# Kernel tuning notes

Measured on AMD Instinct MI355X. Metric: run time of the kernel, lower is better.

## Reference

```python
import jax, jax.numpy as jnp
import numpy as np

DIM = 1024
DEPTH = 4
D_STATE = 16
D_CONV = 4
D_INNER = 2 * DIM
DT_RANK = (DIM + 15) // 16  # 64, ceil(dim/16) as in mamba-ssm
B_SZ, L = 4, 2048


def setup_inputs() -> dict:
    key = jax.random.key(0)
    ks = jax.random.split(key, 10)
    s = 0.02
    x = jax.random.normal(ks[0], (B_SZ, L, DIM), jnp.float32)
    in_proj_w = jax.random.normal(ks[1], (DEPTH, 2 * D_INNER, DIM), jnp.float32) * s
    conv_w = jax.random.normal(ks[2], (DEPTH, D_INNER, D_CONV), jnp.float32) * 0.2
    conv_b = jnp.zeros((DEPTH, D_INNER), jnp.float32)
    x_proj_w = jax.random.normal(ks[3], (DEPTH, DT_RANK + 2 * D_STATE, D_INNER), jnp.float32) * s
    dt_proj_w = jax.random.normal(ks[4], (DEPTH, D_INNER, DT_RANK), jnp.float32) * s
    # bias init so softplus(bias) ~ 0.01 (mamba dt_init)
    dt_proj_b = jnp.full((DEPTH, D_INNER), float(np.log(np.expm1(0.01))), jnp.float32)
    # S4D-real init: A = -(1..d_state)
    A_log = jnp.broadcast_to(jnp.log(jnp.arange(1, D_STATE + 1, dtype=jnp.float32)), (D_INNER, D_STATE))
    A_log = jnp.broadcast_to(A_log, (DEPTH, D_INNER, D_STATE))
    D = jnp.ones((DEPTH, D_INNER), jnp.float32)
    out_proj_w = jax.random.normal(ks[5], (DEPTH, DIM, D_INNER), jnp.float32) * s
    return {"x": x, "in_proj_w": in_proj_w, "conv_w": conv_w, "conv_b": conv_b,
            "x_proj_w": x_proj_w, "dt_proj_w": dt_proj_w, "dt_proj_b": dt_proj_b,
            "A_log": A_log, "D": D, "out_proj_w": out_proj_w}


def _selective_scan(u, delta, A, Bm, Cm, D):
    # u, delta: [B, L, d_inner]; Bm, Cm: [B, L, d_state]; A: [d_inner, d_state]
    def step(h, inp):
        u_t, d_t, b_t, c_t = inp  # [B,di], [B,di], [B,ds], [B,ds]
        dA = jnp.exp(d_t[:, :, None] * A)                 # [B,di,ds]
        h = dA * h + (d_t * u_t)[:, :, None] * b_t[:, None, :]
        y = jnp.einsum('bds,bs->bd', h, c_t)
        return h, y

    h0 = jnp.zeros((u.shape[0], u.shape[2], A.shape[1]), u.dtype)
    xs = (u.transpose(1, 0, 2), delta.transpose(1, 0, 2),
          Bm.transpose(1, 0, 2), Cm.transpose(1, 0, 2))
    _, ys = jax.lax.scan(step, h0, xs)                     # ys: [L,B,di]
    return ys.transpose(1, 0, 2) + u * D


def _mamba_layer(x, in_w, cw, cb, xp_w, dtw, dtb, A_log, D, ow):
    xz = jnp.einsum('bld,ed->ble', x, in_w)               # [B,L,2*di]
    xi, z = jnp.split(xz, 2, axis=-1)
    # causal depthwise conv over L
    xc = jax.lax.conv_general_dilated(
        xi.transpose(0, 2, 1),                             # [B,di,L]
        cw[:, None, :],                                    # [di,1,k]
        window_strides=(1,), padding=[(D_CONV - 1, 0)],
        feature_group_count=D_INNER,
        dimension_numbers=('NCH', 'OIH', 'NCH'))
    xc = jax.nn.silu(xc.transpose(0, 2, 1) + cb)           # [B,L,di]
    dbc = jnp.einsum('bld,ed->ble', xc, xp_w)              # [B,L,dt_rank+2*ds]
    dt, Bm, Cm = jnp.split(dbc, [DT_RANK, DT_RANK + D_STATE], axis=-1)
    delta = jax.nn.softplus(jnp.einsum('blr,dr->bld', dt, dtw) + dtb)
    A = -jnp.exp(A_log)
    y = _selective_scan(xc, delta, A, Bm, Cm, D)
    y = y * jax.nn.silu(z)
    return jnp.einsum('bld,od->blo', y, ow)


def reference(x, in_proj_w, conv_w, conv_b, x_proj_w, dt_proj_w, dt_proj_b, A_log, D, out_proj_w):
    for i in range(DEPTH):
        x = _mamba_layer(x, in_proj_w[i], conv_w[i], conv_b[i], x_proj_w[i],
                         dt_proj_w[i], dt_proj_b[i], A_log[i], D[i], out_proj_w[i])
    return x
```

## Files before the change

kernel.cpp:

```cpp
#include <hip/hip_runtime.h>
#include <hip/hip_bf16.h>
#include <math.h>

#define DIMK 1024
#define NDEPTH 4
#define DS 16
#define DCONV 4
#define DI 2048
#define DTR 64
#define NB 4
#define SL 2048
#define MT (NB * SL)
#define NXZ (2 * DI)
#define NDBC (DTR + 2 * DS)

typedef float f32x4 __attribute__((ext_vector_type(4)));
typedef short short8 __attribute__((ext_vector_type(8)));
typedef short short4v __attribute__((ext_vector_type(4)));

__device__ inline unsigned short f2bf(float f) {
    unsigned u = __builtin_bit_cast(unsigned, f);
    unsigned r = (u + 0x7FFFu + ((u >> 16) & 1u)) >> 16;
    return (unsigned short)r;
}
__device__ inline float bf2f(unsigned short h) {
    unsigned u = ((unsigned)h) << 16;
    return __builtin_bit_cast(float, u);
}
__device__ inline void split_bf(float f, unsigned short& hi, unsigned short& lo) {
    hi = f2bf(f);
    lo = f2bf(f - bf2f(hi));
}
__device__ inline unsigned short cvt1(float f) {
    __hip_bfloat16 t = __float2bfloat16(f);
    return __builtin_bit_cast(unsigned short, t);
}
__device__ inline void mfma16(f32x4& d, short8 a, short8 b) {
    asm volatile("v_mfma_f32_16x16x32_bf16 %0, %1, %2, %0"
                 : "+v"(d) : "v"(a), "v"(b));
}
__device__ __forceinline__ float dpp_sum16(float p) {
    asm("v_add_f32_dpp %0, %0, %0 quad_perm:[1,0,3,2] row_mask:0xf bank_mask:0xf bound_ctrl:0" : "+v"(p));
    asm("v_add_f32_dpp %0, %0, %0 quad_perm:[2,3,0,1] row_mask:0xf bank_mask:0xf bound_ctrl:0" : "+v"(p));
    asm("v_add_f32_dpp %0, %0, %0 row_ror:4 row_mask:0xf bank_mask:0xf bound_ctrl:0" : "+v"(p));
    asm("v_add_f32_dpp %0, %0, %0 row_ror:8 row_mask:0xf bank_mask:0xf bound_ctrl:0" : "+v"(p));
    return p;
}
__device__ __forceinline__ float exp2_raw(float x) {
    float r;
    asm("v_exp_f32 %0, %1" : "=v"(r) : "v"(x));
    return r;
}
__device__ __forceinline__ void gload16(const unsigned short* g, unsigned short* l) {
    __builtin_amdgcn_global_load_lds(
        (const __attribute__((address_space(1))) unsigned int*)(g),
        (__attribute__((address_space(3))) unsigned int*)(l),
        16, 0, 0);
}

__global__ __launch_bounds__(256) void cvt_bf16(
    const float* __restrict__ s, unsigned short* __restrict__ d, int n4)
{
    const int g = blockIdx.x * 256 + threadIdx.x;
    if (g < n4) {
        const float4 f = *(const float4*)(s + (size_t)g * 4);
        short4v v;
        v[0] = (short)cvt1(f.x); v[1] = (short)cvt1(f.y);
        v[2] = (short)cvt1(f.z); v[3] = (short)cvt1(f.w);
        *(short4v*)(d + (size_t)g * 4) = v;
    }
}

__global__ __launch_bounds__(256) void cvt_layer(
    const float* __restrict__ wi, const float* __restrict__ owp,
    const float* __restrict__ dtwp, const float* __restrict__ xpwp,
    unsigned short* __restrict__ wi16, unsigned short* __restrict__ ow16,
    unsigned short* __restrict__ dtwh, unsigned short* __restrict__ dtwl,
    unsigned short* __restrict__ xpwh, unsigned short* __restrict__ xpwl,
    int fastd, int fastx)
{
    int g = blockIdx.x * 256 + threadIdx.x;
    const int n4w = NXZ * DIMK / 4;
    const int n4o = DIMK * DI / 4;
    const int n4d = DI * DTR / 4;
    const int n4x = NDBC * DI / 4;
    if (g < n4w) {
        const float4 f = *(const float4*)(wi + (size_t)g * 4);
        short4v v;
        v[0] = (short)cvt1(f.x); v[1] = (short)cvt1(f.y);
        v[2] = (short)cvt1(f.z); v[3] = (short)cvt1(f.w);
        *(short4v*)(wi16 + (size_t)g * 4) = v;
        return;
    }
    g -= n4w;
    if (g < n4o) {
        const float4 f = *(const float4*)(owp + (size_t)g * 4);
        short4v v;
        v[0] = (short)cvt1(f.x); v[1] = (short)cvt1(f.y);
        v[2] = (short)cvt1(f.z); v[3] = (short)cvt1(f.w);
        *(short4v*)(ow16 + (size_t)g * 4) = v;
        return;
    }
    g -= n4o;
    if (g < n4d) {
        if (fastd) {
            const float4 f = *(const float4*)(dtwp + (size_t)g * 4);
            short4v h4, l4;
            #pragma unroll
            for (int e = 0; e < 4; ++e) {
                unsigned short h, l;
                split_bf((&f.x)[e], h, l);
                h4[e] = (short)h; l4[e] = (short)l;
            }
            *(short4v*)(dtwh + (size_t)g * 4) = h4;
            *(short4v*)(dtwl + (size_t)g * 4) = l4;
        }
        return;
    }
    g -= n4d;
    if (g < n4x && fastx) {
        const float4 f = *(const float4*)(xpwp + (size_t)g * 4);
        short4v h4, l4;
        #pragma unroll
        for (int e = 0; e < 4; ++e) {
            unsigned short h, l;
            split_bf((&f.x)[e], h, l);
            h4[e] = (short)h; l4[e] = (short)l;
        }
        *(short4v*)(xpwh + (size_t)g * 4) = h4;
        *(short4v*)(xpwl + (size_t)g * 4) = l4;
    }
}

__global__ __launch_bounds__(256) void cvt_all(
    const float* __restrict__ wi, const float* __restrict__ owp,
    const float* __restrict__ dtwp, const float* __restrict__ xpwp,
    unsigned short* __restrict__ wi16, unsigned short* __restrict__ ow16,
    unsigned short* __restrict__ dtwh, unsigned short* __restrict__ dtwl,
    unsigned short* __restrict__ xpwh, unsigned short* __restrict__ xpwl)
{
    const int n4w = NXZ * DIMK / 4;
    const int n4o = DIMK * DI / 4;
    const int n4d = DI * DTR / 4;
    const int n4x = NDBC * DI / 4;
    const int per = n4w + n4o + n4d + n4x;
    int g = blockIdx.x * 256 + threadIdx.x;
    const int ly = g / per;
    if (ly >= NDEPTH) return;
    g -= ly * per;
    if (g < n4w) {
        const float4 f = *(const float4*)(wi + (size_t)ly * NXZ * DIMK + (size_t)g * 4);
        short4v v;
        v[0] = (short)cvt1(f.x); v[1] = (short)cvt1(f.y);
        v[2] = (short)cvt1(f.z); v[3] = (short)cvt1(f.w);
        *(short4v*)(wi16 + (size_t)ly * NXZ * DIMK + (size_t)g * 4) = v;
        return;
    }
    g -= n4w;
    if (g < n4o) {
        const float4 f = *(const float4*)(owp + (size_t)ly * DIMK * DI + (size_t)g * 4);
        short4v v;
        v[0] = (short)cvt1(f.x); v[1] = (short)cvt1(f.y);
        v[2] = (short)cvt1(f.z); v[3] = (short)cvt1(f.w);
        *(short4v*)(ow16 + (size_t)ly * DIMK * DI + (size_t)g * 4) = v;
        return;
    }
    g -= n4o;
    if (g < n4d) {
        const float4 f = *(const float4*)(dtwp + (size_t)ly * DI * DTR + (size_t)g * 4);
        short4v h4, l4;
        #pragma unroll
        for (int e = 0; e < 4; ++e) {
            unsigned short h, l;
            split_bf((&f.x)[e], h, l);
            h4[e] = (short)h; l4[e] = (short)l;
        }
        *(short4v*)(dtwh + (size_t)ly * DI * DTR + (size_t)g * 4) = h4;
        *(short4v*)(dtwl + (size_t)ly * DI * DTR + (size_t)g * 4) = l4;
        return;
    }
    g -= n4d;
    if (g < n4x) {
        const float4 f = *(const float4*)(xpwp + (size_t)ly * NDBC * DI + (size_t)g * 4);
        short4v h4, l4;
        #pragma unroll
        for (int e = 0; e < 4; ++e) {
            unsigned short h, l;
            split_bf((&f.x)[e], h, l);
            h4[e] = (short)h; l4[e] = (short)l;
        }
        *(short4v*)(xpwh + (size_t)ly * NDBC * DI + (size_t)g * 4) = h4;
        *(short4v*)(xpwl + (size_t)ly * NDBC * DI + (size_t)g * 4) = l4;
    }
}

template <int CBF>
__global__ __launch_bounds__(256) void gemm_bb(
    const unsigned short* __restrict__ A, const unsigned short* __restrict__ B,
    void* __restrict__ Cv, int K, int lda, int ldb, int ldc)
{
    __shared__ unsigned short As[128 * 32];
    __shared__ unsigned short Bs[128 * 32];
    int id = blockIdx.y * gridDim.x + blockIdx.x;
    const int qq = (gridDim.x * gridDim.y) >> 3;
    id = (id & 7) * qq + (id >> 3);
    const int bm = (id / gridDim.x) * 128, bn = (id % gridDim.x) * 128;

    const int tid = threadIdx.x;
    const int wv = tid >> 6, ln = tid & 63;
    const int wr = wv >> 1, wc = wv & 1;
    const int fr = ln & 15, kg = ln >> 4;
    const int sr0 = wv * 32 + (ln >> 2);
    const int sr1 = sr0 + 16;
    const int sl = ln & 3;
    const int cg0 = sl ^ ((sr0 >> 1) & 3);
    const int cg1 = sl ^ ((sr1 >> 1) & 3);
    const unsigned short* pa0 = A + (size_t)(bm + sr0) * lda + cg0 * 8;
    const unsigned short* pa1 = A + (size_t)(bm + sr1) * lda + cg1 * 8;
    const unsigned short* pb0 = B + (size_t)(bn + sr0) * ldb + cg0 * 8;
    const unsigned short* pb1 = B + (size_t)(bn + sr1) * ldb + cg1 * 8;
    unsigned short* la0 = As + (wv * 32 + 0) * 32;
    unsigned short* la1 = As + (wv * 32 + 16) * 32;
    unsigned short* lb0 = Bs + (wv * 32 + 0) * 32;
    unsigned short* lb1 = Bs + (wv * 32 + 16) * 32;
    int offA[4], offB[4];
    #pragma unroll
    for (int f = 0; f < 4; ++f) {
        const int ra = wr * 64 + f * 16 + fr;
        offA[f] = ra * 32 + ((kg ^ ((ra >> 1) & 3)) * 8);
        const int rb = wc * 64 + f * 16 + fr;
        offB[f] = rb * 32 + ((kg ^ ((rb >> 1) & 3)) * 8);
    }
    f32x4 acc[4][4] = {};
    for (int k0 = 0; k0 < K; k0 += 32) {
        gload16(pa0 + k0, la0);
        gload16(pa1 + k0, la1);
        gload16(pb0 + k0, lb0);
        gload16(pb1 + k0, lb1);
        __syncthreads();
        short8 af[4], bw[4];
        #pragma unroll
        for (int f = 0; f < 4; ++f) {
            af[f] = *(const short8*)&As[offA[f]];
            bw[f] = *(const short8*)&Bs[offB[f]];
        }
        #pragma unroll
        for (int fi = 0; fi < 4; ++fi)
            #pragma unroll
            for (int fj = 0; fj < 4; ++fj)
                mfma16(acc[fi][fj], af[fi], bw[fj]);
        __syncthreads();
    }
    #pragma unroll
    for (int fi = 0; fi < 4; ++fi) {
        const int m0 = bm + wr * 64 + fi * 16 + kg * 4;
        #pragma unroll
        for (int fj = 0; fj < 4; ++fj) {
            const int n = bn + wc * 64 + fj * 16 + fr;
            #pragma unroll
            for (int q = 0; q < 4; ++q) {
                if (CBF) {
                    unsigned short* Cs = (unsigned short*)Cv;
                    Cs[(size_t)(m0 + q) * ldc + n] = cvt1(acc[fi][fj][q]);
                } else {
                    float* Cf = (float*)Cv;
                    Cf[(size_t)(m0 + q) * ldc + n] = acc[fi][fj][q];
                }
            }
        }
    }
}

template <int CBF>
__global__ __launch_bounds__(256) void gemm_fb(
    const float* __restrict__ A, const unsigned short* __restrict__ B,
    void* __restrict__ Cv, int K, int lda, int ldb, int ldc)
{
    __shared__ unsigned short As[2][128 * 32];
    __shared__ unsigned short Bs[2][128 * 32];
    int id = blockIdx.y * gridDim.x + blockIdx.x;
    const int qq = (gridDim.x * gridDim.y) >> 3;
    id = (id & 7) * qq + (id >> 3);
    const int bm = (id / gridDim.x) * 128, bn = (id % gridDim.x) * 128;

    const int tid = threadIdx.x;
    const int wv = tid >> 6, ln = tid & 63;
    const int wr = wv >> 1, wc = wv & 1;
    const int fr = ln & 15, kg = ln >> 4;
    const int r = tid >> 1, hf = tid & 1;
    const int sr0 = wv * 32 + (ln >> 2);
    const int sr1 = sr0 + 16;
    const int sl = ln & 3;
    const int cg0 = sl ^ ((sr0 >> 1) & 3);
    const int cg1 = sl ^ ((sr1 >> 1) & 3);
    const unsigned short* pb0 = B + (size_t)(bn + sr0) * ldb + cg0 * 8;
    const unsigned short* pb1 = B + (size_t)(bn + sr1) * ldb + cg1 * 8;
    const int ldst0 = (wv * 32 + 0) * 32;
    const int ldst1 = (wv * 32 + 16) * 32;
    const float* ga = A + (size_t)(bm + r) * lda + hf * 16;
    const int pk0 = (2 * hf + 0) ^ ((r >> 1) & 3);
    const int pk1 = (2 * hf + 1) ^ ((r >> 1) & 3);
    int offA[4], offB[4];
    #pragma unroll
    for (int f = 0; f < 4; ++f) {
        const int ra = wr * 64 + f * 16 + fr;
        offA[f] = ra * 32 + ((kg ^ ((ra >> 1) & 3)) * 8);
        const int rb = wc * 64 + f * 16 + fr;
        offB[f] = rb * 32 + ((kg ^ ((rb >> 1) & 3)) * 8);
    }
    f32x4 acc[4][4] = {};
    {
        float4 f0 = *(const float4*)(ga + 0);
        float4 f1 = *(const float4*)(ga + 4);
        float4 f2 = *(const float4*)(ga + 8);
        float4 f3 = *(const float4*)(ga + 12);
        short8 v;
        v[0] = (short)cvt1(f0.x); v[1] = (short)cvt1(f0.y);
        v[2] = (short)cvt1(f0.z); v[3] = (short)cvt1(f0.w);
        v[4] = (short)cvt1(f1.x); v[5] = (short)cvt1(f1.y);
        v[6] = (short)cvt1(f1.z); v[7] = (short)cvt1(f1.w);
        *(short8*)&As[0][r * 32 + pk0 * 8] = v;
        v[0] = (short)cvt1(f2.x); v[1] = (short)cvt1(f2.y);
        v[2] = (short)cvt1(f2.z); v[3] = (short)cvt1(f2.w);
        v[4] = (short)cvt1(f3.x); v[5] = (short)cvt1(f3.y);
        v[6] = (short)cvt1(f3.z); v[7] = (short)cvt1(f3.w);
        *(short8*)&As[0][r * 32 + pk1 * 8] = v;
        gload16(pb0, &Bs[0][ldst0]);
        gload16(pb1, &Bs[0][ldst1]);
    }
    __syncthreads();
    int cur = 0;
    for (int k0 = 0; k0 < K; k0 += 32) {
        const int nxt = cur ^ 1;
        const bool more = (k0 + 32 < K);
        float4 f0, f1, f2, f3;
        if (more) {
            gload16(pb0 + k0 + 32, &Bs[nxt][ldst0]);
            gload16(pb1 + k0 + 32, &Bs[nxt][ldst1]);
            f0 = *(const float4*)(ga + k0 + 32);
            f1 = *(const float4*)(ga + k0 + 36);
            f2 = *(const float4*)(ga + k0 + 40);
            f3 = *(const float4*)(ga + k0 + 44);
        }
        short8 af[4], bw[4];
        #pragma unroll
        for (int f = 0; f < 4; ++f) {
            af[f] = *(const short8*)&As[cur][offA[f]];
            bw[f] = *(const short8*)&Bs[cur][offB[f]];
        }
        #pragma unroll
        for (int fi = 0; fi < 4; ++fi)
            #pragma unroll
            for (int fj = 0; fj < 4; ++fj)
                mfma16(acc[fi][fj], af[fi], bw[fj]);
        if (more) {
            short8 v;
            v[0] = (short)cvt1(f0.x); v[1] = (short)cvt1(f0.y);
            v[2] = (short)cvt1(f0.z); v[3] = (short)cvt1(f0.w);
            v[4] = (short)cvt1(f1.x); v[5] = (short)cvt1(f1.y);
            v[6] = (short)cvt1(f1.z); v[7] = (short)cvt1(f1.w);
            *(short8*)&As[nxt][r * 32 + pk0 * 8] = v;
            v[0] = (short)cvt1(f2.x); v[1] = (short)cvt1(f2.y);
            v[2] = (short)cvt1(f2.z); v[3] = (short)cvt1(f2.w);
            v[4] = (short)cvt1(f3.x); v[5] = (short)cvt1(f3.y);
            v[6] = (short)cvt1(f3.z); v[7] = (short)cvt1(f3.w);
            *(short8*)&As[nxt][r * 32 + pk1 * 8] = v;
        }
        __syncthreads();
        cur = nxt;
    }
    #pragma unroll
    for (int fi = 0; fi < 4; ++fi) {
        const int m0 = bm + wr * 64 + fi * 16 + kg * 4;
        #pragma unroll
        for (int fj = 0; fj < 4; ++fj) {
            const int n = bn + wc * 64 + fj * 16 + fr;
            #pragma unroll
            for (int q = 0; q < 4; ++q) {
                if (CBF) {
                    unsigned short* Cs = (unsigned short*)Cv;
                    Cs[(size_t)(m0 + q) * ldc + n] = cvt1(acc[fi][fj][q]);
                } else {
                    float* Cf = (float*)Cv;
                    Cf[(size_t)(m0 + q) * ldc + n] = acc[fi][fj][q];
                }
            }
        }
    }
}

__global__ __launch_bounds__(256) void gemm_mfma(
    const float* __restrict__ A, const float* __restrict__ W,
    float* __restrict__ C, int K, int lda, int ldc)
{
    __shared__ unsigned short As[128 * 32];
    __shared__ unsigned short Ws[128 * 32];
    const int tid = threadIdx.x;
    const int bm = blockIdx.y * 128;
    const int bn = blockIdx.x * 128;
    const int r = tid >> 1;
    const int h = tid & 1;
    const int wv = tid >> 6;
    const int wr = wv >> 1;
    const int wc = wv & 1;
    const int ln = tid & 63;
    const int fr = ln & 15;
    const int kg = ln >> 4;
    f32x4 acc[4][4] = {};
    const float* ga = A + (size_t)(bm + r) * lda + h * 16;
    const float* gw = W + (size_t)(bn + r) * K + h * 16;
    for (int k0 = 0; k0 < K; k0 += 32) {
        #pragma unroll
        for (int p = 0; p < 2; ++p) {
            const int pk = (2 * h + p) ^ ((r >> 1) & 3);
            float4 f0 = *(const float4*)(ga + k0 + p * 8);
            float4 f1 = *(const float4*)(ga + k0 + p * 8 + 4);
            short8 v;
            v[0] = (short)cvt1(f0.x); v[1] = (short)cvt1(f0.y);
            v[2] = (short)cvt1(f0.z); v[3] = (short)cvt1(f0.w);
            v[4] = (short)cvt1(f1.x); v[5] = (short)cvt1(f1.y);
            v[6] = (short)cvt1(f1.z); v[7] = (short)cvt1(f1.w);
            *(short8*)&As[r * 32 + pk * 8] = v;
            f0 = *(const float4*)(gw + k0 + p * 8);
            f1 = *(const float4*)(gw + k0 + p * 8 + 4);
            v[0] = (short)cvt1(f0.x); v[1] = (short)cvt1(f0.y);
            v[2] = (short)cvt1(f0.z); v[3] = (short)cvt1(f0.w);
            v[4] = (short)cvt1(f1.x); v[5] = (short)cvt1(f1.y);
            v[6] = (short)cvt1(f1.z); v[7] = (short)cvt1(f1.w);
            *(short8*)&Ws[r * 32 + pk * 8] = v;
        }
        __syncthreads();
        short8 af[4], bw[4];
        #pragma unroll
        for (int f = 0; f < 4; ++f) {
            const int ra = wr * 64 + f * 16 + fr;
            af[f] = *(const short8*)&As[ra * 32 + ((kg ^ ((ra >> 1) & 3)) * 8)];
            const int rb = wc * 64 + f * 16 + fr;
            bw[f] = *(const short8*)&Ws[rb * 32 + ((kg ^ ((rb >> 1) & 3)) * 8)];
        }
        #pragma unroll
        for (int fi = 0; fi < 4; ++fi)
            #pragma unroll
            for (int fj = 0; fj < 4; ++fj)
                mfma16(acc[fi][fj], af[fi], bw[fj]);
        __syncthreads();
    }
    #pragma unroll
    for (int fi = 0; fi < 4; ++fi) {
        const int m0 = bm + wr * 64 + fi * 16 + kg * 4;
        #pragma unroll
        for (int fj = 0; fj < 4; ++fj) {
            const int n = bn + wc * 64 + fj * 16 + fr;
            #pragma unroll
            for (int q = 0; q < 4; ++q)
                C[(size_t)(m0 + q) * ldc + n] = acc[fi][fj][q];
        }
    }
}

__global__ __launch_bounds__(256) void gemm_xproj_pre(
    const unsigned short* __restrict__ Ahg, const unsigned short* __restrict__ Alg,
    const unsigned short* __restrict__ Whg, const unsigned short* __restrict__ Wlg,
    float* __restrict__ C,
    unsigned short* __restrict__ dth, unsigned short* __restrict__ dtl)
{
    __shared__ unsigned short Ahs[2][128 * 32], Als[2][128 * 32];
    __shared__ unsigned short Whs[2][32 * 32], Wls[2][32 * 32];
    int id = blockIdx.y * gridDim.x + blockIdx.x;
    const int qq = (gridDim.x * gridDim.y) >> 3;
    id = (id & 7) * qq + (id >> 3);
    const int bm = (id / gridDim.x) * 128, bn = (id % gridDim.x) * 32;

    const int tid = threadIdx.x;
    const int wv = tid >> 6, ln = tid & 63;
    const int fr = ln & 15, kg = ln >> 4;
    const int sr0 = wv * 32 + (ln >> 2);
    const int sr1 = sr0 + 16;
    const int sl = ln & 3;
    const int cg0 = sl ^ ((sr0 >> 1) & 3);
    const int cg1 = sl ^ ((sr1 >> 1) & 3);
    const unsigned short* pah0 = Ahg + (size_t)(bm + sr0) * DI + cg0 * 8;
    const unsigned short* pah1 = Ahg + (size_t)(bm + sr1) * DI + cg1 * 8;
    const unsigned short* pal0 = Alg + (size_t)(bm + sr0) * DI + cg0 * 8;
    const unsigned short* pal1 = Alg + (size_t)(bm + sr1) * DI + cg1 * 8;
    const int lA0 = (wv * 32 + 0) * 32;
    const int lA1 = (wv * 32 + 16) * 32;
    const int wrow = (wv & 1) * 16 + (ln >> 2);
    const int cgw = sl ^ ((wrow >> 1) & 3);
    const unsigned short* pw = ((wv < 2) ? Whg : Wlg) + (size_t)(bn + wrow) * DI + cgw * 8;
    const int lW = ((wv & 1) * 16) * 32;
    unsigned short* wdst[2];
    wdst[0] = (wv < 2) ? &Whs[0][lW] : &Wls[0][lW];
    wdst[1] = (wv < 2) ? &Whs[1][lW] : &Wls[1][lW];

    int offA[2], offW[2];
    #pragma unroll
    for (int f = 0; f < 2; ++f) {
        const int ra = wv * 32 + f * 16 + fr;
        offA[f] = ra * 32 + ((kg ^ ((ra >> 1) & 3)) * 8);
        const int rb = f * 16 + fr;
        offW[f] = rb * 32 + ((kg ^ ((rb >> 1) & 3)) * 8);
    }
    f32x4 acc[2][2] = {};
    gload16(pah0, &Ahs[0][lA0]);
    gload16(pah1, &Ahs[0][lA1]);
    gload16(pal0, &Als[0][lA0]);
    gload16(pal1, &Als[0][lA1]);
    gload16(pw, wdst[0]);
    __syncthreads();
    int cur = 0;
    for (int k0 = 0; k0 < DI; k0 += 32) {
        const int nxt = cur ^ 1;
        if (k0 + 32 < DI) {
            gload16(pah0 + k0 + 32, &Ahs[nxt][lA0]);
            gload16(pah1 + k0 + 32, &Ahs[nxt][lA1]);
            gload16(pal0 + k0 + 32, &Als[nxt][lA0]);
            gload16(pal1 + k0 + 32, &Als[nxt][lA1]);
            gload16(pw + k0 + 32, wdst[nxt]);
        }
        short8 ah[2], alo[2], bh[2], bl[2];
        #pragma unroll
        for (int f = 0; f < 2; ++f) {
            ah[f]  = *(const short8*)&Ahs[cur][offA[f]];
            alo[f] = *(const short8*)&Als[cur][offA[f]];
            bh[f]  = *(const short8*)&Whs[cur][offW[f]];
            bl[f]  = *(const short8*)&Wls[cur][offW[f]];
        }
        #pragma unroll
        for (int fi = 0; fi < 2; ++fi)
            #pragma unroll
            for (int fj = 0; fj < 2; ++fj) {
                mfma16(acc[fi][fj], ah[fi], bh[fj]);
                mfma16(acc[fi][fj], ah[fi], bl[fj]);
                mfma16(acc[fi][fj], alo[fi], bh[fj]);
            }
        __syncthreads();
        cur = nxt;
    }
    #pragma unroll
    for (int fi = 0; fi < 2; ++fi) {
        const int m0 = bm + wv * 32 + fi * 16 + kg * 4;
        #pragma unroll
        for (int fj = 0; fj < 2; ++fj) {
            const int n = bn + fj * 16 + fr;
            #pragma unroll
            for (int q = 0; q < 4; ++q) {
                const float v = acc[fi][fj][q];
                C[(size_t)(m0 + q) * NDBC + n] = v;
                if (n < DTR) {
                    unsigned short hh, llo;
                    split_bf(v, hh, llo);
                    dth[(size_t)(m0 + q) * DTR + n] = hh;
                    dtl[(size_t)(m0 + q) * DTR + n] = llo;
                }
            }
        }
    }
}

template <int WRDT>
__global__ __launch_bounds__(256) void gemm_xproj(
    const float* __restrict__ A, const float* __restrict__ W,
    float* __restrict__ C, int K, int lda,
    unsigned short* __restrict__ dth, unsigned short* __restrict__ dtl)
{
    __shared__ unsigned short Ah[128 * 32], Al[128 * 32];
    __shared__ unsigned short Wh[32 * 32], Wl[32 * 32];
    const int tid = threadIdx.x;
    const int bm = blockIdx.y * 128;
    const int bn = blockIdx.x * 32;
    const int r = tid >> 1, hf = tid & 1;
    const int wv = tid >> 6;
    const int ln = tid & 63, fr = ln & 15, kg = ln >> 4;
    const int wsr = tid >> 3;
    const int wc4 = (tid & 7) << 2;
    f32x4 acc[2][2] = {};
    const float* ga = A + (size_t)(bm + r) * lda + hf * 16;
    const float* gw = W + (size_t)(bn + wsr) * K + wc4;
    for (int k0 = 0; k0 < K; k0 += 32) {
        #pragma unroll
        for (int j = 0; j < 4; ++j) {
            const int col = hf * 16 + j * 4;
            const int ad = r * 32 + (((col >> 3) ^ ((r >> 1) & 3)) << 3) + (col & 7);
            const float4 fa = *(const float4*)(ga + k0 + j * 4);
            short4v h4, l4;
            #pragma unroll
            for (int e = 0; e < 4; ++e) {
                unsigned short hh, llo;
                split_bf((&fa.x)[e], hh, llo);
                h4[e] = (short)hh; l4[e] = (short)llo;
            }
            *(short4v*)&Ah[ad] = h4;
            *(short4v*)&Al[ad] = l4;
        }
        {
            const int ad = wsr * 32 + (((wc4 >> 3) ^ ((wsr >> 1) & 3)) << 3) + (wc4 & 7);
            const float4 fw = *(const float4*)(gw + k0);
            short4v h4, l4;
            #pragma unroll
            for (int e = 0; e < 4; ++e) {
                unsigned short hh, llo;
                split_bf((&fw.x)[e], hh, llo);
                h4[e] = (short)hh; l4[e] = (short)llo;
            }
            *(short4v*)&Wh[ad] = h4;
            *(short4v*)&Wl[ad] = l4;
        }
        __syncthreads();
        short8 ah[2], alo[2], bh[2], bl[2];
        #pragma unroll
        for (int f = 0; f < 2; ++f) {
            const int ra = wv * 32 + f * 16 + fr;
            const int ao = ra * 32 + ((kg ^ ((ra >> 1) & 3)) * 8);
            ah[f]  = *(const short8*)&Ah[ao];
            alo[f] = *(const short8*)&Al[ao];
            const int rb = f * 16 + fr;
            const int bo = rb * 32 + ((kg ^ ((rb >> 1) & 3)) * 8);
            bh[f] = *(const short8*)&Wh[bo];
            bl[f] = *(const short8*)&Wl[bo];
        }
        #pragma unroll
        for (int fi = 0; fi < 2; ++fi)
            #pragma unroll
            for (int fj = 0; fj < 2; ++fj) {
                mfma16(acc[fi][fj], ah[fi], bh[fj]);
                mfma16(acc[fi][fj], ah[fi], bl[fj]);
                mfma16(acc[fi][fj], alo[fi], bh[fj]);
            }
        __syncthreads();
    }
    #pragma unroll
    for (int fi = 0; fi < 2; ++fi) {
        const int m0 = bm + wv * 32 + fi * 16 + kg * 4;
        #pragma unroll
        for (int fj = 0; fj < 2; ++fj) {
            const int n = bn + fj * 16 + fr;
            #pragma unroll
            for (int q = 0; q < 4; ++q) {
                const float v = acc[fi][fj][q];
                C[(size_t)(m0 + q) * NDBC + n] = v;
                if (WRDT && n < DTR) {
                    unsigned short hh, llo;
                    split_bf(v, hh, llo);
                    dth[(size_t)(m0 + q) * DTR + n] = hh;
                    dtl[(size_t)(m0 + q) * DTR + n] = llo;
                }
            }
        }
    }
}

__global__ __launch_bounds__(256) void gemm_delta(
    const float* __restrict__ A, const float* __restrict__ W,
    float* __restrict__ C, const float* __restrict__ bias)
{
    __shared__ unsigned short Ah[128 * 32], Al[128 * 32];
    __shared__ unsigned short Wh[128 * 32], Wl[128 * 32];
    const int tid = threadIdx.x;
    const int bm = blockIdx.y * 128;
    const int bn = blockIdx.x * 128;
    const int r = tid >> 1, hf = tid & 1;
    const int wv = tid >> 6, wr = wv >> 1, wc = wv & 1;
    const int ln = tid & 63, fr = ln & 15, kg = ln >> 4;
    f32x4 acc[4][4] = {};
    const float* ga = A + (size_t)(bm + r) * NDBC + hf * 16;
    const float* gw = W + (size_t)(bn + r) * DTR + hf * 16;
    for (int k0 = 0; k0 < DTR; k0 += 32) {
        #pragma unroll
        for (int j = 0; j < 4; ++j) {
            const int col = hf * 16 + j * 4;
            const int ad = r * 32 + (((col >> 3) ^ ((r >> 1) & 3)) << 3) + (col & 7);
            const float4 fa = *(const float4*)(ga + k0 + j * 4);
            const float4 fw = *(const float4*)(gw + k0 + j * 4);
            short4v ah4, al4, wh4, wl4;
            #pragma unroll
            for (int e = 0; e < 4; ++e) {
                unsigned short hh, llo;
                split_bf((&fa.x)[e], hh, llo);
                ah4[e] = (short)hh; al4[e] = (short)llo;
                split_bf((&fw.x)[e], hh, llo);
                wh4[e] = (short)hh; wl4[e] = (short)llo;
            }
            *(short4v*)&Ah[ad] = ah4; *(short4v*)&Al[ad] = al4;
            *(short4v*)&Wh[ad] = wh4; *(short4v*)&Wl[ad] = wl4;
        }
        __syncthreads();
        short8 ah[4], alo[4], bh[4], bl[4];
        #pragma unroll
        for (int f = 0; f < 4; ++f) {
            const int ra = wr * 64 + f * 16 + fr;
            const int ao = ra * 32 + ((kg ^ ((ra >> 1) & 3)) * 8);
            ah[f]  = *(const short8*)&Ah[ao];
            alo[f] = *(const short8*)&Al[ao];
            const int rb = wc * 64 + f * 16 + fr;
            const int bo = rb * 32 + ((kg ^ ((rb >> 1) & 3)) * 8);
            bh[f] = *(const short8*)&Wh[bo];
            bl[f] = *(const short8*)&Wl[bo];
        }
        #pragma unroll
        for (int fi = 0; fi < 4; ++fi)
            #pragma unroll
            for (int fj = 0; fj < 4; ++fj) {
                mfma16(acc[fi][fj], ah[fi], bh[fj]);
                mfma16(acc[fi][fj], ah[fi], bl[fj]);
                mfma16(acc[fi][fj], alo[fi], bh[fj]);
            }
        __syncthreads();
    }
    #pragma unroll
    for (int fi = 0; fi < 4; ++fi) {
        const int m0 = bm + wr * 64 + fi * 16 + kg * 4;
        #pragma unroll
        for (int fj = 0; fj < 4; ++fj) {
            const int n = bn + wc * 64 + fj * 16 + fr;
            const float bb = bias[n];
            #pragma unroll
            for (int q = 0; q < 4; ++q) {
                float v = acc[fi][fj][q] + bb;
                v = (v > 20.f) ? v : log1pf(__expf(v));
                C[(size_t)(m0 + q) * NXZ + n] = v;
            }
        }
    }
}

__global__ __launch_bounds__(256) void gemm_delta_pre(
    const unsigned short* __restrict__ Ahg, const unsigned short* __restrict__ Alg,
    const unsigned short* __restrict__ Whg, const unsigned short* __restrict__ Wlg,
    float* __restrict__ C, const float* __restrict__ bias)
{
    __shared__ unsigned short sAh[128 * 64], sAl[128 * 64];
    __shared__ unsigned short sWh[128 * 64], sWl[128 * 64];
    const int tid = threadIdx.x;
    const int bm = blockIdx.y * 128;
    const int bn = blockIdx.x * 128;
    const int wv = tid >> 6, ln = tid & 63;
    const int wr = wv >> 1, wc = wv & 1;
    const int fr = ln & 15, kg = ln >> 4;
    const int srow = ln >> 3;
    const int g = ln & 7;
    const int half = g >> 2, sub = g & 3;
    #pragma unroll
    for (int j = 0; j < 4; ++j) {
        const int row = wv * 32 + j * 8 + srow;
        const int sub2 = sub ^ ((row >> 1) & 3);
        const int scol = half * 32 + sub2 * 8;
        const int dst = (wv * 32 + j * 8) * 64;
        gload16(Ahg + (size_t)(bm + row) * DTR + scol, sAh + dst);
        gload16(Alg + (size_t)(bm + row) * DTR + scol, sAl + dst);
        gload16(Whg + (size_t)(bn + row) * DTR + scol, sWh + dst);
        gload16(Wlg + (size_t)(bn + row) * DTR + scol, sWl + dst);
    }
    __syncthreads();
    f32x4 acc[4][4] = {};
    #pragma unroll
    for (int ks = 0; ks < 2; ++ks) {
        short8 ah[4], alo[4], bh[4], bl[4];
        #pragma unroll
        for (int f = 0; f < 4; ++f) {
            const int ra = wr * 64 + f * 16 + fr;
            const int ao = ra * 64 + ks * 32 + ((kg ^ ((ra >> 1) & 3)) * 8);
            ah[f]  = *(const short8*)&sAh[ao];
            alo[f] = *(const short8*)&sAl[ao];
            const int rb = wc * 64 + f * 16 + fr;
            const int bo = rb * 64 + ks * 32 + ((kg ^ ((rb >> 1) & 3)) * 8);
            bh[f] = *(const short8*)&sWh[bo];
            bl[f] = *(const short8*)&sWl[bo];
        }
        #pragma unroll
        for (int fi = 0; fi < 4; ++fi)
            #pragma unroll
            for (int fj = 0; fj < 4; ++fj) {
                mfma16(acc[fi][fj], ah[fi], bh[fj]);
                mfma16(acc[fi][fj], ah[fi], bl[fj]);
                mfma16(acc[fi][fj], alo[fi], bh[fj]);
            }
    }
    #pragma unroll
    for (int fi = 0; fi < 4; ++fi) {
        const int m0 = bm + wr * 64 + fi * 16 + kg * 4;
        #pragma unroll
        for (int fj = 0; fj < 4; ++fj) {
            const int n = bn + wc * 64 + fj * 16 + fr;
            const float bb = bias[n];
            #pragma unroll
            for (int q = 0; q < 4; ++q) {
                float v = acc[fi][fj][q] + bb;
                v = (v > 20.f) ? v : log1pf(__expf(v));
                C[(size_t)(m0 + q) * NXZ + n] = v;
            }
        }
    }
}

__global__ __launch_bounds__(256) void conv_silu(
    const float* __restrict__ xz, const float* __restrict__ cw,
    const float* __restrict__ cb, float* __restrict__ xc)
{
    const int g = blockIdx.x * 256 + threadIdx.x;
    const int c4 = g & (DI / 4 - 1);
    const int mq = g >> 9;
    const int m0 = mq << 2;
    const int l0 = m0 & (SL - 1);
    const int c = c4 << 2;
    const float4 w0 = *(const float4*)(cw + (size_t)(c + 0) * DCONV);
    const float4 w1 = *(const float4*)(cw + (size_t)(c + 1) * DCONV);
    const float4 w2 = *(const float4*)(cw + (size_t)(c + 2) * DCONV);
    const float4 w3 = *(const float4*)(cw + (size_t)(c + 3) * DCONV);
    const float4 cb4 = *(const float4*)(cb + c);
    float4 x[7];
    #pragma unroll
    for (int i = 0; i < 7; ++i) {
        if (l0 - 3 + i >= 0)
            x[i] = *(const float4*)(xz + (size_t)(m0 - 3 + i) * NXZ + c);
        else
            x[i] = make_float4(0.f, 0.f, 0.f, 0.f);
    }
    #pragma unroll
    for (int j = 0; j < 4; ++j) {
        float4 acc = cb4;
        #pragma unroll
        for (int k = 0; k < DCONV; ++k) {
            const float4 v = x[j + k];
            acc.x = fmaf(v.x, (&w0.x)[k], acc.x);
            acc.y = fmaf(v.y, (&w1.x)[k], acc.y);
            acc.z = fmaf(v.z, (&w2.x)[k], acc.z);
            acc.w = fmaf(v.w, (&w3.x)[k], acc.w);
        }
        acc.x = acc.x / (1.f + __expf(-acc.x));
        acc.y = acc.y / (1.f + __expf(-acc.y));
        acc.z = acc.z / (1.f + __expf(-acc.z));
        acc.w = acc.w / (1.f + __expf(-acc.w));
        *(float4*)(xc + (size_t)(m0 + j) * DI + c) = acc;
    }
}

__global__ __launch_bounds__(256) void conv_silu_split(
    const float* __restrict__ xz, const float* __restrict__ cw,
    const float* __restrict__ cb, unsigned short* __restrict__ xch,
    unsigned short* __restrict__ xcl)
{
    const int g = blockIdx.x * 256 + threadIdx.x;
    const int c4 = g & (DI / 4 - 1);
    const int mq = g >> 9;
    const int m0 = mq << 2;
    const int l0 = m0 & (SL - 1);
    const int c = c4 << 2;
    const float4 w0 = *(const float4*)(cw + (size_t)(c + 0) * DCONV);
    const float4 w1 = *(const float4*)(cw + (size_t)(c + 1) * DCONV);
    const float4 w2 = *(const float4*)(cw + (size_t)(c + 2) * DCONV);
    const float4 w3 = *(const float4*)(cw + (size_t)(c + 3) * DCONV);
    const float4 cb4 = *(const float4*)(cb + c);
    float4 x[7];
    #pragma unroll
    for (int i = 0; i < 7; ++i) {
        if (l0 - 3 + i >= 0)
            x[i] = *(const float4*)(xz + (size_t)(m0 - 3 + i) * NXZ + c);
        else
            x[i] = make_float4(0.f, 0.f, 0.f, 0.f);
    }
    #pragma unroll
    for (int j = 0; j < 4; ++j) {
        float4 acc = cb4;
        #pragma unroll
        for (int k = 0; k < DCONV; ++k) {
            const float4 v = x[j + k];
            acc.x = fmaf(v.x, (&w0.x)[k], acc.x);
            acc.y = fmaf(v.y, (&w1.x)[k], acc.y);
            acc.z = fmaf(v.z, (&w2.x)[k], acc.z);
            acc.w = fmaf(v.w, (&w3.x)[k], acc.w);
        }
        short4v h4, l4;
        #pragma unroll
        for (int e = 0; e < 4; ++e) {
            float a = (&acc.x)[e];
            a = a / (1.f + __expf(-a));
            unsigned short hh, llo;
            split_bf(a, hh, llo);
            h4[e] = (short)hh; l4[e] = (short)llo;
        }
        *(short4v*)(xch + (size_t)(m0 + j) * DI + c) = h4;
        *(short4v*)(xcl + (size_t)(m0 + j) * DI + c) = l4;
    }
}

template <int YBF, int UBF>
__global__ __launch_bounds__(256) void scan_k(
    const float* uf, const unsigned short* __restrict__ uh,
    const unsigned short* __restrict__ ul,
    const float* __restrict__ dbc,
    const float* __restrict__ xz, void* __restrict__ yv,
    const float* __restrict__ Alog, const float* __restrict__ Dl)
{
    const int b = blockIdx.y;
    const int c0 = blockIdx.x * 16;
    const int tid = threadIdx.x;
    const int ch = tid >> 4;
    const int s = tid & 15;
    const float Aa = -__expf(Alog[(size_t)(c0 + ch) * DS + s]) * 1.44269504088896f;
    __shared__ float sdl[2][16][68];
    __shared__ float sxb[2][16][68];
    __shared__ float sbc[2][32][68];
    __shared__ float sy[2][64][16];
    __shared__ float sD[16];
    if (tid < 16) sD[tid] = Dl[c0 + tid];
    float h = 0.f;
    const int row = tid >> 2;
    const int q = (tid & 3) << 2;
    const size_t base = (size_t)b * SL;
    const int r2a = tid >> 3, q2a = (tid & 7) << 2;
    const int r2b = 32 + (tid >> 3);

    float4 dlv, zv, g0, g1, uvf;
    short4v uh4, ul4;
    {
        const size_t m = base + row;
        dlv = *(const float4*)(xz + m * NXZ + c0 + q);
        if (UBF) {
            uh4 = *(const short4v*)(uh + m * DI + c0 + q);
            ul4 = *(const short4v*)(ul + m * DI + c0 + q);
        } else {
            uvf = *(const float4*)(uf + m * DI + c0 + q);
        }
        zv = *(const float4*)(xz + m * NXZ + DI + c0 + q);
        g0 = *(const float4*)(dbc + (base + r2a) * NDBC + DTR + q2a);
        g1 = *(const float4*)(dbc + (base + r2b) * NDBC + DTR + q2a);
    }
    float4 p0c, p1c, p0p, p1p;
    int pp = 0;
    __syncthreads();
    const int NT = SL / 64;
    for (int tile = 0; tile < NT; ++tile) {
        const int buf = tile & 1;
        float4 uv;
        if (UBF) {
            #pragma unroll
            for (int e = 0; e < 4; ++e)
                (&uv.x)[e] = bf2f((unsigned short)uh4[e]) +
                             bf2f((unsigned short)ul4[e]);
        } else uv = uvf;
        #pragma unroll
        for (int j = 0; j < 4; ++j) {
            const float dl = (&dlv.x)[j], uu = (&uv.x)[j], zz = (&zv.x)[j];
            const float w = zz / (1.f + __expf(-zz));
            sdl[buf][q + j][row] = dl;
            sxb[buf][q + j][row] = dl * uu;
            (&p1c.x)[j] = w;
            (&p0c.x)[j] = uu * sD[q + j] * w;
        }
        sbc[buf][q2a + 0][r2a] = g0.x; sbc[buf][q2a + 1][r2a] = g0.y;
        sbc[buf][q2a + 2][r2a] = g0.z; sbc[buf][q2a + 3][r2a] = g0.w;
        sbc[buf][q2a + 0][r2b] = g1.x; sbc[buf][q2a + 1][r2b] = g1.y;
        sbc[buf][q2a + 2][r2b] = g1.z; sbc[buf][q2a + 3][r2b] = g1.w;
        __syncthreads();
        if (tile > 0) {
            const size_t mp = base + (size_t)(tile - 1) * 64 + row;
            if (YBF) {
                unsigned short* y16 = (unsigned short*)yv;
                short4v s4;
                #pragma unroll
                for (int e = 0; e < 4; ++e)
                    s4[e] = (short)cvt1(fmaf(sy[pp ^ 1][row][q + e],
                                             (&p1p.x)[e], (&p0p.x)[e]));
                *(short4v*)(y16 + mp * DI + c0 + q) = s4;
            } else {
                float* y = (float*)yv;
                float4 yvv;
                #pragma unroll
                for (int e = 0; e < 4; ++e)
                    (&yvv.x)[e] = fmaf(sy[pp ^ 1][row][q + e],
                                       (&p1p.x)[e], (&p0p.x)[e]);
                *(float4*)(y + mp * DI + c0 + q) = yvv;
            }
        }
        if (tile + 1 < NT) {
            const size_t m = base + (size_t)(tile + 1) * 64 + row;
            dlv = *(const float4*)(xz + m * NXZ + c0 + q);
            if (UBF) {
                uh4 = *(const short4v*)(uh + m * DI + c0 + q);
                ul4 = *(const short4v*)(ul + m * DI + c0 + q);
            } else {
                uvf = *(const float4*)(uf + m * DI + c0 + q);
            }
            zv = *(const float4*)(xz + m * NXZ + DI + c0 + q);
            const size_t mb2 = base + (size_t)(tile + 1) * 64;
            g0 = *(const float4*)(dbc + (mb2 + r2a) * NDBC + DTR + q2a);
            g1 = *(const float4*)(dbc + (mb2 + r2b) * NDBC + DTR + q2a);
        }
        for (int it = 0; it < 16; ++it) {
            const int t0 = it * 4;
            const float4 dl4 = *(const float4*)&sdl[buf][ch][t0];
            const float4 xb4 = *(const float4*)&sxb[buf][ch][t0];
            const float4 B4  = *(const float4*)&sbc[buf][s][t0];
            const float4 C4  = *(const float4*)&sbc[buf][16 + s][t0];
            float py0, py1, py2, py3;
            {
                const float dA = exp2_raw(dl4.x * Aa);
                h = fmaf(dA, h, xb4.x * B4.x);
                py0 = dpp_sum16(h * C4.x);
            }
            {
                const float dA = exp2_raw(dl4.y * Aa);
                h = fmaf(dA, h, xb4.y * B4.y);
                py1 = dpp_sum16(h * C4.y);
            }
            {
                const float dA = exp2_raw(dl4.z * Aa);
                h = fmaf(dA, h, xb4.z * B4.z);
                py2 = dpp_sum16(h * C4.z);
            }
            {
                const float dA = exp2_raw(dl4.w * Aa);
                h = fmaf(dA, h, xb4.w * B4.w);
                py3 = dpp_sum16(h * C4.w);
            }
            if (s < 4) {
                const int t = t0 + s;
                const float lo_ = (s & 1) ? py1 : py0;
                const float hi_ = (s & 1) ? py3 : py2;
                sy[pp][t][ch] = (s & 2) ? hi_ : lo_;
            }
        }
        p0p = p0c; p1p = p1c;
        pp ^= 1;
    }
    __syncthreads();
    {
        const size_t mp = base + (size_t)(NT - 1) * 64 + row;
        if (YBF) {
            unsigned short* y16 = (unsigned short*)yv;
            short4v s4;
            #pragma unroll
            for (int e = 0; e < 4; ++e)
                s4[e] = (short)cvt1(fmaf(sy[pp ^ 1][row][q + e],
                                         (&p1p.x)[e], (&p0p.x)[e]));
            *(short4v*)(y16 + mp * DI + c0 + q) = s4;
        } else {
            float* y = (float*)yv;
            float4 yvv;
            #pragma unroll
            for (int e = 0; e < 4; ++e)
                (&yvv.x)[e] = fmaf(sy[pp ^ 1][row][q + e],
                                   (&p1p.x)[e], (&p0p.x)[e]);
            *(float4*)(y + mp * DI + c0 + q) = yvv;
        }
    }
}

extern "C" void kernel_launch(void* const* d_in, const int* in_sizes, int n_in,
                              void* d_out, int out_size, void* d_ws, size_t ws_size,
                              hipStream_t stream)
{
    const float* x0   = (const float*)d_in[0];
    const float* in_w = (const float*)d_in[1];
    const float* cw   = (const float*)d_in[2];
    const float* cb   = (const float*)d_in[3];
    const float* xpw  = (const float*)d_in[4];
    const float* dtw  = (const float*)d_in[5];
    const float* dtb  = (const float*)d_in[6];
    const float* Alog = (const float*)d_in[7];
    const float* Dp   = (const float*)d_in[8];
    const float* ow   = (const float*)d_in[9];

    const size_t perB = (size_t)SL * (NXZ + DI + NDBC) * sizeof(float);
    const size_t wby  = ((size_t)NXZ * DIMK + (size_t)DIMK * DI) * 2;
    int nbc = 0, fast = 0;
    if (ws_size >= 4 * perB + wby)      { nbc = 4; fast = 1; }
    else if (ws_size >= 2 * perB + wby) { nbc = 2; fast = 1; }
    else if (ws_size >= perB + wby)     { nbc = 1; fast = 1; }
    else if (ws_size >= 4 * perB)       { nbc = 4; }
    else if (ws_size >= 2 * perB)       { nbc = 2; }
    else if (ws_size >= perB)           { nbc = 1; }
    else return;
    const int nchunks = NB / nbc;
    const int M = nbc * SL;
    const size_t dtby = ((size_t)DI * DTR * 2 + (size_t)M * DTR * 2) * 2;
    const size_t yby  = (size_t)M * DI * 2;
    const size_t xpby = (size_t)NDBC * DI * 2 * 2;
    const size_t base = (size_t)nbc * perB + wby;
    const int fastd = fast && (ws_size >= base + dtby);
    const int fasty = fastd && (ws_size >= base + dtby + yby);
    const int fastx = fasty && (ws_size >= base + dtby + yby + xpby);
    const size_t wAll = ((size_t)NDEPTH * NXZ * DIMK + (size_t)NDEPTH * DIMK * DI +
                         2 * (size_t)NDEPTH * DI * DTR + 2 * (size_t)NDEPTH * NDBC * DI) * 2;
    const size_t chunkBy = (size_t)nbc * perB;
    const int fastw = fastx &&
        (ws_size >= chunkBy + wAll + (size_t)M * DTR * 2 * 2 + yby);

    float* xz  = (float*)d_ws;
    float* xc  = xz + (size_t)M * NXZ;
    float* dbc = xc + (size_t)M * DI;
    unsigned short* xch = (unsigned short*)xc;
    unsigned short* xcl = xch + (size_t)M * DI;

    unsigned short* p = (unsigned short*)(dbc + (size_t)M * NDBC);
    unsigned short *wi16, *ow16, *dtwh, *dtwl, *xpwh, *xpwl, *dth, *dtl, *y16;
    size_t wiStride = 0, owStride = 0, dtwStride = 0, xpwStride = 0;
    if (fastw) {
        wi16 = p;                    p += (size_t)NDEPTH * NXZ * DIMK;
        ow16 = p;                    p += (size_t)NDEPTH * DIMK * DI;
        dtwh = p;                    p += (size_t)NDEPTH * DI * DTR;
        dtwl = p;                    p += (size_t)NDEPTH * DI * DTR;
        xpwh = p;                    p += (size_t)NDEPTH * NDBC * DI;
        xpwl = p;                    p += (size_t)NDEPTH * NDBC * DI;
        wiStride = (size_t)NXZ * DIMK; owStride = (size_t)DIMK * DI;
        dtwStride = (size_t)DI * DTR;  xpwStride = (size_t)NDBC * DI;
    } else {
        wi16 = p;                    p += (size_t)NXZ * DIMK;
        ow16 = p;                    p += (size_t)DIMK * DI;
        dtwh = p;                    p += (size_t)DI * DTR;
        dtwl = p;                    p += (size_t)DI * DTR;
        xpwh = nullptr; xpwl = nullptr;
    }
    dth = p;                         p += (size_t)M * DTR;
    dtl = p;                         p += (size_t)M * DTR;
    y16 = p;                         p += (size_t)M * DI;
    if (!fastw && fastx) { xpwh = p; p += (size_t)NDBC * DI; xpwl = p; }

    unsigned short* xb16 = (unsigned short*)d_out + (size_t)MT * DIMK;
    float* xbuf = (float*)d_out;

    const dim3 blk(256);
    if (fastx) {
        const int n4x0 = MT * DIMK / 4;
        cvt_bf16<<<dim3(n4x0 / 256), blk, 0, stream>>>(x0, xb16, n4x0);
    }
    if (fastw) {
        const int per = (NXZ * DIMK / 4) + (DIMK * DI / 4) + (DI * DTR / 4) +
                        (NDBC * DI / 4);
        cvt_all<<<dim3((NDEPTH * per + 255) / 256), blk, 0, stream>>>(
            in_w, ow, dtw, xpw, wi16, ow16, dtwh, dtwl, xpwh, xpwl);
    }
    const int ncv = (NXZ * DIMK / 4) + (DIMK * DI / 4) + (DI * DTR / 4) +
                    (NDBC * DI / 4);
    for (int ly = 0; ly < NDEPTH; ++ly) {
        const float* Wi   = in_w + (size_t)ly * NXZ * DIMK;
        const float* cwl  = cw   + (size_t)ly * DI * DCONV;
        const float* cbl  = cb   + (size_t)ly * DI;
        const float* xpl  = xpw  + (size_t)ly * NDBC * DI;
        const float* dtwl_ = dtw + (size_t)ly * DI * DTR;
        const float* dtbl = dtb  + (size_t)ly * DI;
        const float* Al   = Alog + (size_t)ly * DI * DS;
        const float* Dl   = Dp   + (size_t)ly * DI;
        const float* owl  = ow   + (size_t)ly * DIMK * DI;

        const unsigned short* wi16L = wi16 + (size_t)ly * wiStride;
        const unsigned short* ow16L = ow16 + (size_t)ly * owStride;
        const unsigned short* dtwhL = dtwh + (size_t)ly * dtwStride;
        const unsigned short* dtwlL = dtwl + (size_t)ly * dtwStride;
        const unsigned short* xpwhL = fastx ? xpwh + (size_t)ly * xpwStride : nullptr;
        const unsigned short* xpwlL = fastx ? xpwl + (size_t)ly * xpwStride : nullptr;

        if (fast && !fastw)
            cvt_layer<<<dim3((ncv + 255) / 256), blk, 0, stream>>>(
                Wi, owl, dtwl_, xpl, wi16, ow16, dtwh, dtwl,
                (unsigned short*)xpwh, (unsigned short*)xpwl, fastd, fastx);

        for (int ck = 0; ck < nchunks; ++ck) {
            if (fastx) {
                const unsigned short* xin16 = xb16 + (size_t)ck * M * DIMK;
                gemm_bb<0><<<dim3(NXZ / 128, M / 128), blk, 0, stream>>>(
                    xin16, wi16L, xz, DIMK, DIMK, DIMK, NXZ);
                conv_silu_split<<<dim3(M * (DI / 16) / 256), blk, 0, stream>>>(
                    xz, cwl, cbl, xch, xcl);
                gemm_xproj_pre<<<dim3(3, M / 128), blk, 0, stream>>>(
                    xch, xcl, xpwhL, xpwlL, dbc, dth, dtl);
                gemm_delta_pre<<<dim3(DI / 128, M / 128), blk, 0, stream>>>(
                    dth, dtl, dtwhL, dtwlL, xz, dtbl);
                scan_k<1, 1><<<dim3(DI / 16, nbc), blk, 0, stream>>>(
                    nullptr, xch, xcl, dbc, xz, y16, Al, Dl);
                void* dst = (ly < NDEPTH - 1)
                    ? (void*)(xb16 + (size_t)ck * M * DIMK)
                    : (void*)((float*)d_out + (size_t)ck * M * DIMK);
                if (ly < NDEPTH - 1)
                    gemm_bb<1><<<dim3(DIMK / 128, M / 128), blk, 0, stream>>>(
                        y16, ow16L, dst, DI, DI, DI, DIMK);
                else
                    gemm_bb<0><<<dim3(DIMK / 128, M / 128), blk, 0, stream>>>(
                        y16, ow16L, dst, DI, DI, DI, DIMK);
            } else if (fast) {
                if (ly == 0) {
                    const float* xin = x0 + (size_t)ck * M * DIMK;
                    gemm_fb<0><<<dim3(NXZ / 128, M / 128), blk, 0, stream>>>(
                        xin, wi16, xz, DIMK, DIMK, DIMK, NXZ);
                } else {
                    const unsigned short* xin16 = xb16 + (size_t)ck * M * DIMK;
                    gemm_bb<0><<<dim3(NXZ / 128, M / 128), blk, 0, stream>>>(
                        xin16, wi16, xz, DIMK, DIMK, DIMK, NXZ);
                }
                conv_silu<<<dim3(M * (DI / 16) / 256), blk, 0, stream>>>(
                    xz, cwl, cbl, xc);
                if (fastd) {
                    gemm_xproj<1><<<dim3(3, M / 128), blk, 0, stream>>>(
                        xc, xpl, dbc, DI, DI, dth, dtl);
                    gemm_delta_pre<<<dim3(DI / 128, M / 128), blk, 0, stream>>>(
                        dth, dtl, dtwh, dtwl, xz, dtbl);
                } else {
                    gemm_xproj<0><<<dim3(3, M / 128), blk, 0, stream>>>(
                        xc, xpl, dbc, DI, DI, nullptr, nullptr);
                    gemm_delta<<<dim3(DI / 128, M / 128), blk, 0, stream>>>(
                        dbc, dtwl_, xz, dtbl);
                }
                void* dst = (ly < NDEPTH - 1)
                    ? (void*)(xb16 + (size_t)ck * M * DIMK)
                    : (void*)((float*)d_out + (size_t)ck * M * DIMK);
                if (fasty) {
                    scan_k<1, 0><<<dim3(DI / 16, nbc), blk, 0, stream>>>(
                        xc, nullptr, nullptr, dbc, xz, y16, Al, Dl);
                    if (ly < NDEPTH - 1)
                        gemm_bb<1><<<dim3(DIMK / 128, M / 128), blk, 0, stream>>>(
                            y16, ow16, dst, DI, DI, DI, DIMK);
                    else
                        gemm_bb<0><<<dim3(DIMK / 128, M / 128), blk, 0, stream>>>(
                            y16, ow16, dst, DI, DI, DI, DIMK);
                } else {
                    scan_k<0, 0><<<dim3(DI / 16, nbc), blk, 0, stream>>>(
                        xc, nullptr, nullptr, dbc, xz, xc, Al, Dl);
                    if (ly < NDEPTH - 1)
                        gemm_fb<1><<<dim3(DIMK / 128, M / 128), blk, 0, stream>>>(
                            xc, ow16, dst, DI, DI, DI, DIMK);
                    else
                        gemm_fb<0><<<dim3(DIMK / 128, M / 128), blk, 0, stream>>>(
                            xc, ow16, dst, DI, DI, DI, DIMK);
                }
            } else {
                const float* xin = (ly == 0 ? x0 : xbuf) + (size_t)ck * M * DIMK;
                gemm_mfma<<<dim3(NXZ / 128, M / 128), blk, 0, stream>>>(
                    xin, Wi, xz, DIMK, DIMK, NXZ);
                conv_silu<<<dim3(M * (DI / 16) / 256), blk, 0, stream>>>(
                    xz, cwl, cbl, xc);
                gemm_xproj<0><<<dim3(3, M / 128), blk, 0, stream>>>(
                    xc, xpl, dbc, DI, DI, nullptr, nullptr);
                gemm_delta<<<dim3(DI / 128, M / 128), blk, 0, stream>>>(
                    dbc, dtwl_, xz, dtbl);
                scan_k<0, 0><<<dim3(DI / 16, nbc), blk, 0, stream>>>(
                    xc, nullptr, nullptr, dbc, xz, xc, Al, Dl);
                float* xdst = (ly == NDEPTH - 1 ? (float*)d_out : xbuf) +
                              (size_t)ck * M * DIMK;
                gemm_mfma<<<dim3(DIMK / 128, M / 128), blk, 0, stream>>>(
                    xc, owl, xdst, DI, DI, DIMK);
            }
        }
    }
}
```

Baseline: 1.597 ms.

## Triple-buffer LDS tiles in bf16 GEMM with async prefetch two stages ahead

Replaces the single-buffered LDS load/sync/compute loop in the bf16 MFMA GEMM with a three-stage ring buffer. Global-to-LDS loads for tile t+2 are issued while tile t is being multiplied. Explicit vmcnt waits and one barrier per iteration replace the two __syncthreads. This is meant to hide global memory latency behind the MFMAs, at the cost of three times the LDS per block, which may lower occupancy.

```diff
diff --git a/kernel.cpp b/kernel.cpp
--- a/kernel.cpp
+++ b/kernel.cpp
@@ -199,8 +199,8 @@
     const unsigned short* __restrict__ A, const unsigned short* __restrict__ B,
     void* __restrict__ Cv, int K, int lda, int ldb, int ldc)
 {
-    __shared__ unsigned short As[128 * 32];
-    __shared__ unsigned short Bs[128 * 32];
+    __shared__ unsigned short As[3][128 * 32];
+    __shared__ unsigned short Bs[3][128 * 32];
     int id = blockIdx.y * gridDim.x + blockIdx.x;
     const int qq = (gridDim.x * gridDim.y) >> 3;
     id = (id & 7) * qq + (id >> 3);
@@ -219,10 +219,8 @@
     const unsigned short* pa1 = A + (size_t)(bm + sr1) * lda + cg1 * 8;
     const unsigned short* pb0 = B + (size_t)(bn + sr0) * ldb + cg0 * 8;
     const unsigned short* pb1 = B + (size_t)(bn + sr1) * ldb + cg1 * 8;
-    unsigned short* la0 = As + (wv * 32 + 0) * 32;
-    unsigned short* la1 = As + (wv * 32 + 16) * 32;
-    unsigned short* lb0 = Bs + (wv * 32 + 0) * 32;
-    unsigned short* lb1 = Bs + (wv * 32 + 16) * 32;
+    const int ldst0 = (wv * 32 + 0) * 32;
+    const int ldst1 = (wv * 32 + 16) * 32;
     int offA[4], offB[4];
     #pragma unroll
     for (int f = 0; f < 4; ++f) {
@@ -232,24 +230,41 @@
         offB[f] = rb * 32 + ((kg ^ ((rb >> 1) & 3)) * 8);
     }
     f32x4 acc[4][4] = {};
-    for (int k0 = 0; k0 < K; k0 += 32) {
-        gload16(pa0 + k0, la0);
-        gload16(pa1 + k0, la1);
-        gload16(pb0 + k0, lb0);
-        gload16(pb1 + k0, lb1);
-        __syncthreads();
+    const int NT = K >> 5;
+    gload16(pa0, &As[0][ldst0]);
+    gload16(pa1, &As[0][ldst1]);
+    gload16(pb0, &Bs[0][ldst0]);
+    gload16(pb1, &Bs[0][ldst1]);
+    gload16(pa0 + 32, &As[1][ldst0]);
+    gload16(pa1 + 32, &As[1][ldst1]);
+    gload16(pb0 + 32, &Bs[1][ldst0]);
+    gload16(pb1 + 32, &Bs[1][ldst1]);
+    int cur = 0, wrb = 2;
+    for (int t = 0; t < NT; ++t) {
+        if (t + 1 < NT) asm volatile("s_waitcnt vmcnt(4)" ::: "memory");
+        else            asm volatile("s_waitcnt vmcnt(0)" ::: "memory");
+        __builtin_amdgcn_s_barrier();
+        __builtin_amdgcn_sched_barrier(0);
         short8 af[4], bw[4];
         #pragma unroll
         for (int f = 0; f < 4; ++f) {
-            af[f] = *(const short8*)&As[offA[f]];
-            bw[f] = *(const short8*)&Bs[offB[f]];
+            af[f] = *(const short8*)&As[cur][offA[f]];
+            bw[f] = *(const short8*)&Bs[cur][offB[f]];
         }
         #pragma unroll
         for (int fi = 0; fi < 4; ++fi)
             #pragma unroll
             for (int fj = 0; fj < 4; ++fj)
                 mfma16(acc[fi][fj], af[fi], bw[fj]);
-        __syncthreads();
+        if (t + 2 < NT) {
+            const int k2 = (t + 2) * 32;
+            gload16(pa0 + k2, &As[wrb][ldst0]);
+            gload16(pa1 + k2, &As[wrb][ldst1]);
+            gload16(pb0 + k2, &Bs[wrb][ldst0]);
+            gload16(pb1 + k2, &Bs[wrb][ldst1]);
+        }
+        cur = (cur == 2) ? 0 : cur + 1;
+        wrb = (wrb == 2) ? 0 : wrb + 1;
     }
     #pragma unroll
     for (int fi = 0; fi < 4; ++fi) {
```

New measurement: 1.628 ms. About the same (+2.0%).
